# Optimization experiments

Measured on AMD Instinct MI355X. Metric: run time of the kernel, lower is better.

Reference implementation:

```python
import jax, jax.numpy as jnp
import numpy as np


def setup_inputs() -> dict:
    key = jax.random.key(0)
    ks = jax.random.split(key, 5)
    B, T, D, U = 32, 2048, 512, 512
    scale = 1.0 / np.sqrt(D)
    return {
        "full": jax.random.normal(ks[0], (B, T, D), jnp.float32),
        "last": jax.random.normal(ks[1], (B, D), jnp.float32),
        "W1": jax.random.normal(ks[2], (D, U), jnp.float32) * scale,
        "b1": jnp.zeros((U,), jnp.float32),
        "W2": jax.random.normal(ks[3], (D, U), jnp.float32) * scale,
        "b2": jnp.zeros((U,), jnp.float32),
        "V": jax.random.normal(ks[4], (U, 1), jnp.float32) * (1.0 / np.sqrt(U)),
        "bV": jnp.zeros((1,), jnp.float32),
    }


def reference(full, last, W1, b1, W2, b2, V, bV):
    # full: [B,T,D], last: [B,D]
    h1 = jnp.einsum("btd,du->btu", full, W1) + b1          # [B,T,U]
    h2 = last @ W2 + b2                                      # [B,U]
    score = jnp.tanh(h1 + h2[:, None, :]) @ V + bV           # [B,T,1]
    attn = jax.nn.softmax(score, axis=1)                     # [B,T,1]
    context = jnp.sum(attn * full, axis=1)                   # [B,D]
    return context
```

## Files before the change

### kernel.cpp

```cpp
#include <hip/hip_runtime.h>
#include <math.h>


#define BB 32
#define TT 2048
#define DD 512
#define UU 512
#define BKK 32
#define KSTEPS 16

typedef short bf16x8 __attribute__((ext_vector_type(8)));
typedef float f32x4  __attribute__((ext_vector_type(4)));

static __device__ __forceinline__ short f2bf(float f) {
    unsigned x = __float_as_uint(f);
    return (short)((x + 0x7fffu + ((x >> 16) & 1u)) >> 16);
}

static __device__ __forceinline__ float fast_tanh(float x) {
    float e = __expf(2.f * x);
    return 1.f - 2.f * __builtin_amdgcn_rcpf(e + 1.f);
}

__global__ __launch_bounds__(256) void prep_kernel(const float* __restrict__ W1,
                                                   short* __restrict__ W1T,
                                                   const float* __restrict__ last,
                                                   const float* __restrict__ W2,
                                                   const float* __restrict__ b1,
                                                   const float* __restrict__ b2,
                                                   float* __restrict__ h2) {
    __shared__ float tile[32][33];
    __shared__ float ls[DD];
    __shared__ float part[256];
    const int bid = blockIdx.x;
    const int tid = threadIdx.x;
    if (bid < 256) {
        const int tr = (bid >> 4) << 5;
        const int tc = (bid & 15) << 5;
#pragma unroll
        for (int p = 0; p < 4; ++p) {
            const int r = p * 8 + (tid >> 5), c = tid & 31;
            tile[r][c] = W1[(size_t)(tr + r) * UU + tc + c];
        }
        __syncthreads();
#pragma unroll
        for (int p = 0; p < 4; ++p) {
            const int r = p * 8 + (tid >> 5), c = tid & 31;
            W1T[(size_t)(tc + r) * DD + tr + c] = f2bf(tile[c][r]);
        }
    } else {
        const int b2i = bid - 256;
        const int b  = b2i >> 2;
        const int u0 = (b2i & 3) << 7;
        for (int i = tid; i < DD; i += 256) ls[i] = last[b * DD + i];
        __syncthreads();
        const int uu = tid & 127;
        const int dh = tid >> 7;
        float acc = 0.f;
#pragma unroll 8
        for (int d = dh * 256; d < dh * 256 + 256; ++d)
            acc += ls[d] * W2[d * UU + u0 + uu];
        part[tid] = acc;
        __syncthreads();
        if (tid < 128) {
            const int u = u0 + tid;
            h2[b * UU + u] = part[tid] + part[tid + 128] + b1[u] + b2[u];
        }
    }
}

__global__ __launch_bounds__(512) void score_kernel(const float* __restrict__ full,
                                                    const short* __restrict__ W1T,
                                                    const float* __restrict__ h2,
                                                    const float* __restrict__ V,
                                                    float* __restrict__ ctx,
                                                    float* __restrict__ m_arr,
                                                    float* __restrict__ l_arr) {
    __shared__ __align__(16) float a32[2][128 * BKK];
    __shared__ __align__(16) short blds[2][512 * BKK];
    __shared__ float red64[8][64];
    __shared__ float esc[128];
    __shared__ float sred[8];
    __shared__ __align__(16) float red4[4][128][4];

    const int bid = blockIdx.x;
    const int b    = bid >> 4;
    const int t0   = (bid & 15) << 7;
    const int tid  = threadIdx.x;
    const int w    = tid >> 6;
    const int lane = tid & 63;
    const int quad = lane >> 4;
    const int col  = lane & 15;
    const int wm   = w >> 2;
    const int wn   = w & 3;

    f32x4 acc[4][8];
#pragma unroll
    for (int i = 0; i < 4; ++i)
#pragma unroll
        for (int j = 0; j < 8; ++j) acc[i][j] = (f32x4){0.f, 0.f, 0.f, 0.f};

    const size_t fullbase = (size_t)(b * TT + t0) * DD;

#define STAGE(bufidx, koidx) do {                                                     \
        _Pragma("unroll")                                                             \
        for (int i = 0; i < 2; ++i) {                                                 \
            const int sb = w * 128 + i * 64;                                          \
            const int s  = sb + lane;                                                 \
            const int r  = s >> 3;                                                    \
            const int cc = (s & 7) ^ (r & 7);                                         \
            const float* g = &full[fullbase + (size_t)r * DD + (koidx) * BKK + cc * 4]; \
            __builtin_amdgcn_global_load_lds(                                         \
                (const __attribute__((address_space(1))) void*)g,                     \
                (__attribute__((address_space(3))) void*)&a32[bufidx][sb * 4], 16, 0, 0); \
        }                                                                             \
        _Pragma("unroll")                                                             \
        for (int i = 0; i < 4; ++i) {                                                 \
            const int sb = w * 256 + i * 64;                                          \
            const int s  = sb + lane;                                                 \
            const int u  = s >> 2;                                                    \
            const int kc = (s & 3) ^ ((u >> 1) & 3);                                  \
            const short* g = &W1T[(size_t)u * DD + (koidx) * BKK + kc * 8];           \
            __builtin_amdgcn_global_load_lds(                                         \
                (const __attribute__((address_space(1))) void*)g,                     \
                (__attribute__((address_space(3))) void*)&blds[bufidx][sb * 8], 16, 0, 0); \
        }                                                                             \
    } while (0)

    STAGE(0, 0);
    STAGE(1, 1);
    asm volatile("s_waitcnt vmcnt(6)" ::: "memory");
    __builtin_amdgcn_s_barrier();

    int cur = 0;
    for (int ko = 0; ko < KSTEPS; ++ko) {
        f32x4 alo[4], ahi[4];
        bf16x8 bfr[8];
#pragma unroll
        for (int mt = 0; mt < 4; ++mt) {
            const int r  = wm * 64 + mt * 16 + col;
            const int c0 = quad * 2;
            alo[mt] = *(const f32x4*)&a32[cur][(r * 8 + (c0 ^ (r & 7))) * 4];
            ahi[mt] = *(const f32x4*)&a32[cur][(r * 8 + ((c0 + 1) ^ (r & 7))) * 4];
        }
#pragma unroll
        for (int nt = 0; nt < 8; ++nt) {
            const int u = wn * 128 + nt * 16 + col;
            bfr[nt] = *(const bf16x8*)&blds[cur][(u * 4 + (quad ^ ((u >> 1) & 3))) * 8];
        }
        asm volatile("s_waitcnt lgkmcnt(0)" ::: "memory");
        __builtin_amdgcn_sched_barrier(0);
        __builtin_amdgcn_s_barrier();

        if (ko + 2 < KSTEPS) STAGE(cur, ko + 2);

        bf16x8 af[4];
#pragma unroll
        for (int mt = 0; mt < 4; ++mt)
            af[mt] = (bf16x8){f2bf(alo[mt].x), f2bf(alo[mt].y), f2bf(alo[mt].z), f2bf(alo[mt].w),
                              f2bf(ahi[mt].x), f2bf(ahi[mt].y), f2bf(ahi[mt].z), f2bf(ahi[mt].w)};
#pragma unroll
        for (int nt = 0; nt < 8; ++nt)
#pragma unroll
            for (int mt = 0; mt < 4; ++mt)
                acc[mt][nt] = __builtin_amdgcn_mfma_f32_16x16x32_bf16(af[mt], bfr[nt], acc[mt][nt], 0, 0, 0);

        if (ko < KSTEPS - 2) {
            asm volatile("s_waitcnt vmcnt(6)" ::: "memory");
        } else if (ko == KSTEPS - 2) {
            asm volatile("s_waitcnt vmcnt(0)" ::: "memory");
        }
        if (ko < KSTEPS - 1) __builtin_amdgcn_s_barrier();
        cur ^= 1;
    }
#undef STAGE

    float srow[16];
#pragma unroll
    for (int i = 0; i < 16; ++i) srow[i] = 0.f;
#pragma unroll
    for (int nt = 0; nt < 8; ++nt) {
        const int u = wn * 128 + nt * 16 + col;
        const float hv = h2[b * UU + u];
        const float vv = V[u];
#pragma unroll
        for (int mt = 0; mt < 4; ++mt)
#pragma unroll
            for (int r = 0; r < 4; ++r)
                srow[mt * 4 + r] += fast_tanh(acc[mt][nt][r] + hv) * vv;
    }
#pragma unroll
    for (int off = 1; off < 16; off <<= 1) {
#pragma unroll
        for (int i = 0; i < 16; ++i) srow[i] += __shfl_xor(srow[i], off, 64);
    }
    if (col == 0) {
#pragma unroll
        for (int mt = 0; mt < 4; ++mt)
#pragma unroll
            for (int r = 0; r < 4; ++r)
                red64[w][mt * 16 + quad * 4 + r] = srow[mt * 4 + r];
    }
    __syncthreads();

    float sv = 0.f;
    if (tid < 128) {
        const int wmX = tid >> 6, rr = tid & 63;
        sv = red64[wmX * 4 + 0][rr] + red64[wmX * 4 + 1][rr] +
             red64[wmX * 4 + 2][rr] + red64[wmX * 4 + 3][rr];
        float mv = sv;
#pragma unroll
        for (int off = 1; off < 64; off <<= 1) mv = fmaxf(mv, __shfl_xor(mv, off, 64));
        if (lane == 0) sred[w] = mv;
    }
    __syncthreads();
    const float M = fmaxf(sred[0], sred[1]);
    if (tid < 128) {
        float e = __expf(sv - M);
        esc[tid] = e;
#pragma unroll
        for (int off = 1; off < 64; off <<= 1) e += __shfl_xor(e, off, 64);
        if (lane == 0) sred[4 + w] = e;
    }
    __syncthreads();
    if (tid == 0) { m_arr[bid] = M; l_arr[bid] = sred[4] + sred[5]; }

    const int c  = tid & 127;
    const int tp = tid >> 7;
    float ax = 0.f, ay = 0.f, az = 0.f, aw = 0.f;
#pragma unroll 4
    for (int i = 0; i < 32; ++i) {
        const int t = i * 4 + tp;
        const float4 v = *(const float4*)&full[fullbase + (size_t)t * DD + c * 4];
        const float e = esc[t];
        ax += e * v.x; ay += e * v.y; az += e * v.z; aw += e * v.w;
    }
    *(float4*)&red4[tp][c][0] = make_float4(ax, ay, az, aw);
    __syncthreads();
    if (tp == 0) {
        const float4 p0 = *(const float4*)&red4[0][c][0];
        const float4 p1 = *(const float4*)&red4[1][c][0];
        const float4 p2 = *(const float4*)&red4[2][c][0];
        const float4 p3 = *(const float4*)&red4[3][c][0];
        float4 s = make_float4(p0.x + p1.x + p2.x + p3.x,
                               p0.y + p1.y + p2.y + p3.y,
                               p0.z + p1.z + p2.z + p3.z,
                               p0.w + p1.w + p2.w + p3.w);
        *(float4*)&ctx[(size_t)bid * DD + c * 4] = s;
    }
}

__global__ __launch_bounds__(256) void combine_kernel(const float* __restrict__ ctx,
                                                      const float* __restrict__ m_arr,
                                                      const float* __restrict__ l_arr,
                                                      float* __restrict__ out) {
    const int b = blockIdx.x;
    const int tid = threadIdx.x;
    __shared__ float wgt[16];
    __shared__ float linv;
    if (tid == 0) {
        float M = -1e30f;
#pragma unroll
        for (int i = 0; i < 16; ++i) M = fmaxf(M, m_arr[b * 16 + i]);
        float l = 0.f;
#pragma unroll
        for (int i = 0; i < 16; ++i) {
            wgt[i] = __expf(m_arr[b * 16 + i] - M);
            l += wgt[i] * l_arr[b * 16 + i];
        }
        linv = 1.f / l;
    }
    __syncthreads();
    float s0 = 0.f, s1 = 0.f;
#pragma unroll
    for (int i = 0; i < 16; ++i) {
        const float wi = wgt[i];
        const float* cp = &ctx[(size_t)(b * 16 + i) * DD + tid * 2];
        s0 += wi * cp[0];
        s1 += wi * cp[1];
    }
    out[b * DD + tid * 2]     = s0 * linv;
    out[b * DD + tid * 2 + 1] = s1 * linv;
}

extern "C" void kernel_launch(void* const* d_in, const int* in_sizes, int n_in,
                              void* d_out, int out_size, void* d_ws, size_t ws_size,
                              hipStream_t stream) {
    const float* full = (const float*)d_in[0];
    const float* last = (const float*)d_in[1];
    const float* W1   = (const float*)d_in[2];
    const float* b1   = (const float*)d_in[3];
    const float* W2   = (const float*)d_in[4];
    const float* b2   = (const float*)d_in[5];
    const float* V    = (const float*)d_in[6];

    float* out   = (float*)d_out;
    float* h2    = (float*)d_ws;
    float* m_arr = h2 + (size_t)BB * UU;
    float* l_arr = m_arr + 512;
    float* ctx   = l_arr + 512;
    short* W1T   = (short*)(ctx + (size_t)BB * 16 * DD);

    prep_kernel<<<384, 256, 0, stream>>>(W1, W1T, last, W2, b1, b2, h2);
    score_kernel<<<BB * 16, 512, 0, stream>>>(full, W1T, h2, V, ctx, m_arr, l_arr);
    combine_kernel<<<BB, 256, 0, stream>>>(ctx, m_arr, l_arr, out);
}
```

Measured before the change: 259.9 us.

## Use 1024-thread blocks with register-staged bf16 A tile conversion

Doubles the score kernel block to 16 waves, each owning a 64x64 output tile instead of 64x128. The A operand (full) is now loaded into registers, converted to bf16 once and written to LDS, rather than copied as fp32 via global_load_lds and converted per wave after the LDS read. The goal is to remove the redundant per-wave conversion, halve A-tile LDS traffic and raise occupancy. In exchange it adds VGPR pressure limits from launch_bounds(1024), more waitcnt and barrier coordination, and register-path global loads for A.

```diff
diff --git a/kernel.cpp b/kernel.cpp
--- a/kernel.cpp
+++ b/kernel.cpp
@@ -10,6 +10,7 @@
 #define KSTEPS 16
 
 typedef short bf16x8 __attribute__((ext_vector_type(8)));
+typedef short s16x4  __attribute__((ext_vector_type(4)));
 typedef float f32x4  __attribute__((ext_vector_type(4)));
 
 static __device__ __forceinline__ short f2bf(float f) {
@@ -69,19 +70,19 @@
     }
 }
 
-__global__ __launch_bounds__(512) void score_kernel(const float* __restrict__ full,
-                                                    const short* __restrict__ W1T,
-                                                    const float* __restrict__ h2,
-                                                    const float* __restrict__ V,
-                                                    float* __restrict__ ctx,
-                                                    float* __restrict__ m_arr,
-                                                    float* __restrict__ l_arr) {
-    __shared__ __align__(16) float a32[2][128 * BKK];
-    __shared__ __align__(16) short blds[2][512 * BKK];
-    __shared__ float red64[8][64];
+__global__ __launch_bounds__(1024, 4) void score_kernel(const float* __restrict__ full,
+                                                        const short* __restrict__ W1T,
+                                                        const float* __restrict__ h2,
+                                                        const float* __restrict__ V,
+                                                        float* __restrict__ ctx,
+                                                        float* __restrict__ m_arr,
+                                                        float* __restrict__ l_arr) {
+    __shared__ __align__(16) short a16[2][128 * 32];
+    __shared__ __align__(16) short blds[2][512 * 32];
+    __shared__ float red64[16][64];
     __shared__ float esc[128];
     __shared__ float sred[8];
-    __shared__ __align__(16) float red4[4][128][4];
+    __shared__ __align__(16) float red4[8][128][4];
 
     const int bid = blockIdx.x;
     const int b    = bid >> 4;
@@ -91,32 +92,26 @@
     const int lane = tid & 63;
     const int quad = lane >> 4;
     const int col  = lane & 15;
-    const int wm   = w >> 2;
-    const int wn   = w & 3;
-
-    f32x4 acc[4][8];
+    const int wm   = w >> 3;
+    const int wn   = w & 7;
+
+    f32x4 acc[4][4];
 #pragma unroll
     for (int i = 0; i < 4; ++i)
 #pragma unroll
-        for (int j = 0; j < 8; ++j) acc[i][j] = (f32x4){0.f, 0.f, 0.f, 0.f};
+        for (int j = 0; j < 4; ++j) acc[i][j] = (f32x4){0.f, 0.f, 0.f, 0.f};
 
     const size_t fullbase = (size_t)(b * TT + t0) * DD;
 
-#define STAGE(bufidx, koidx) do {                                                     \
+    const int sr = tid >> 3;
+    const int se = tid & 7;
+    const float* aSrc = &full[fullbase + (size_t)sr * DD + se * 4];
+    const int awOff = sr * 32 + ((((se >> 1) ^ (sr & 3)) << 3) + ((se & 1) << 2));
+
+#define STAGE_B(bufidx, koidx) do {                                                   \
         _Pragma("unroll")                                                             \
         for (int i = 0; i < 2; ++i) {                                                 \
             const int sb = w * 128 + i * 64;                                          \
-            const int s  = sb + lane;                                                 \
-            const int r  = s >> 3;                                                    \
-            const int cc = (s & 7) ^ (r & 7);                                         \
-            const float* g = &full[fullbase + (size_t)r * DD + (koidx) * BKK + cc * 4]; \
-            __builtin_amdgcn_global_load_lds(                                         \
-                (const __attribute__((address_space(1))) void*)g,                     \
-                (__attribute__((address_space(3))) void*)&a32[bufidx][sb * 4], 16, 0, 0); \
-        }                                                                             \
-        _Pragma("unroll")                                                             \
-        for (int i = 0; i < 4; ++i) {                                                 \
-            const int sb = w * 256 + i * 64;                                          \
             const int s  = sb + lane;                                                 \
             const int u  = s >> 2;                                                    \
             const int kc = (s & 3) ^ ((u >> 1) & 3);                                  \
@@ -127,60 +122,74 @@
         }                                                                             \
     } while (0)
 
-    STAGE(0, 0);
-    STAGE(1, 1);
-    asm volatile("s_waitcnt vmcnt(6)" ::: "memory");
+#define CVT_WRITE(buf, ar) do {                                                       \
+        s16x4 q_ = (s16x4){f2bf((ar).x), f2bf((ar).y), f2bf((ar).z), f2bf((ar).w)};   \
+        *(s16x4*)&a16[buf][awOff] = q_;                                               \
+    } while (0)
+
+    f32x4 aregA = *(const f32x4*)(aSrc + 0 * BKK);
+    f32x4 aregB = *(const f32x4*)(aSrc + 1 * BKK);
+    STAGE_B(0, 0);
+    STAGE_B(1, 1);
+    asm volatile("s_waitcnt vmcnt(5)" ::: "memory");
+    CVT_WRITE(0, aregA);
+    asm volatile("s_waitcnt vmcnt(2)" ::: "memory");
+    asm volatile("s_waitcnt lgkmcnt(0)" ::: "memory");
     __builtin_amdgcn_s_barrier();
 
-    int cur = 0;
     for (int ko = 0; ko < KSTEPS; ++ko) {
-        f32x4 alo[4], ahi[4];
-        bf16x8 bfr[8];
+        const int cur = ko & 1;
+        bf16x8 af[4], bfr[4];
 #pragma unroll
         for (int mt = 0; mt < 4; ++mt) {
-            const int r  = wm * 64 + mt * 16 + col;
-            const int c0 = quad * 2;
-            alo[mt] = *(const f32x4*)&a32[cur][(r * 8 + (c0 ^ (r & 7))) * 4];
-            ahi[mt] = *(const f32x4*)&a32[cur][(r * 8 + ((c0 + 1) ^ (r & 7))) * 4];
-        }
-#pragma unroll
-        for (int nt = 0; nt < 8; ++nt) {
-            const int u = wn * 128 + nt * 16 + col;
+            const int r = wm * 64 + mt * 16 + col;
+            af[mt] = *(const bf16x8*)&a16[cur][r * 32 + ((quad ^ (r & 3)) << 3)];
+        }
+#pragma unroll
+        for (int nt = 0; nt < 4; ++nt) {
+            const int u = wn * 64 + nt * 16 + col;
             bfr[nt] = *(const bf16x8*)&blds[cur][(u * 4 + (quad ^ ((u >> 1) & 3))) * 8];
         }
         asm volatile("s_waitcnt lgkmcnt(0)" ::: "memory");
         __builtin_amdgcn_sched_barrier(0);
         __builtin_amdgcn_s_barrier();
 
-        if (ko + 2 < KSTEPS) STAGE(cur, ko + 2);
-
-        bf16x8 af[4];
-#pragma unroll
-        for (int mt = 0; mt < 4; ++mt)
-            af[mt] = (bf16x8){f2bf(alo[mt].x), f2bf(alo[mt].y), f2bf(alo[mt].z), f2bf(alo[mt].w),
-                              f2bf(ahi[mt].x), f2bf(ahi[mt].y), f2bf(ahi[mt].z), f2bf(ahi[mt].w)};
-#pragma unroll
-        for (int nt = 0; nt < 8; ++nt)
+        if (ko + 1 < KSTEPS) {
+            asm volatile("s_waitcnt vmcnt(2)" ::: "memory");
+            if (ko & 1) CVT_WRITE(cur ^ 1, aregA);
+            else        CVT_WRITE(cur ^ 1, aregB);
+        }
+        if (ko + 2 < KSTEPS) {
+            if (ko & 1) aregB = *(const f32x4*)(aSrc + (ko + 2) * BKK);
+            else        aregA = *(const f32x4*)(aSrc + (ko + 2) * BKK);
+        }
+        if (ko + 2 < KSTEPS) STAGE_B(cur, ko + 2);
+
+#pragma unroll
+        for (int nt = 0; nt < 4; ++nt)
 #pragma unroll
             for (int mt = 0; mt < 4; ++mt)
                 acc[mt][nt] = __builtin_amdgcn_mfma_f32_16x16x32_bf16(af[mt], bfr[nt], acc[mt][nt], 0, 0, 0);
 
         if (ko < KSTEPS - 2) {
-            asm volatile("s_waitcnt vmcnt(6)" ::: "memory");
+            asm volatile("s_waitcnt vmcnt(3)" ::: "memory");
         } else if (ko == KSTEPS - 2) {
             asm volatile("s_waitcnt vmcnt(0)" ::: "memory");
         }
-        if (ko < KSTEPS - 1) __builtin_amdgcn_s_barrier();
-        cur ^= 1;
-    }
-#undef STAGE
+        if (ko < KSTEPS - 1) {
+            asm volatile("s_waitcnt lgkmcnt(0)" ::: "memory");
+            __builtin_amdgcn_s_barrier();
+        }
+    }
+#undef STAGE_B
+#undef CVT_WRITE
 
     float srow[16];
 #pragma unroll
     for (int i = 0; i < 16; ++i) srow[i] = 0.f;
 #pragma unroll
-    for (int nt = 0; nt < 8; ++nt) {
-        const int u = wn * 128 + nt * 16 + col;
+    for (int nt = 0; nt < 4; ++nt) {
+        const int u = wn * 64 + nt * 16 + col;
         const float hv = h2[b * UU + u];
         const float vv = V[u];
 #pragma unroll
@@ -206,8 +215,8 @@
     float sv = 0.f;
     if (tid < 128) {
         const int wmX = tid >> 6, rr = tid & 63;
-        sv = red64[wmX * 4 + 0][rr] + red64[wmX * 4 + 1][rr] +
-             red64[wmX * 4 + 2][rr] + red64[wmX * 4 + 3][rr];
+#pragma unroll
+        for (int j = 0; j < 8; ++j) sv += red64[wmX * 8 + j][rr];
         float mv = sv;
 #pragma unroll
         for (int off = 1; off < 64; off <<= 1) mv = fmaxf(mv, __shfl_xor(mv, off, 64));
@@ -229,8 +238,8 @@
     const int tp = tid >> 7;
     float ax = 0.f, ay = 0.f, az = 0.f, aw = 0.f;
 #pragma unroll 4
-    for (int i = 0; i < 32; ++i) {
-        const int t = i * 4 + tp;
+    for (int i = 0; i < 16; ++i) {
+        const int t = i * 8 + tp;
         const float4 v = *(const float4*)&full[fullbase + (size_t)t * DD + c * 4];
         const float e = esc[t];
         ax += e * v.x; ay += e * v.y; az += e * v.z; aw += e * v.w;
@@ -238,14 +247,12 @@
     *(float4*)&red4[tp][c][0] = make_float4(ax, ay, az, aw);
     __syncthreads();
     if (tp == 0) {
-        const float4 p0 = *(const float4*)&red4[0][c][0];
-        const float4 p1 = *(const float4*)&red4[1][c][0];
-        const float4 p2 = *(const float4*)&red4[2][c][0];
-        const float4 p3 = *(const float4*)&red4[3][c][0];
-        float4 s = make_float4(p0.x + p1.x + p2.x + p3.x,
-                               p0.y + p1.y + p2.y + p3.y,
-                               p0.z + p1.z + p2.z + p3.z,
-                               p0.w + p1.w + p2.w + p3.w);
+        float4 s = make_float4(0.f, 0.f, 0.f, 0.f);
+#pragma unroll
+        for (int j = 0; j < 8; ++j) {
+            const float4 p = *(const float4*)&red4[j][c][0];
+            s.x += p.x; s.y += p.y; s.z += p.z; s.w += p.w;
+        }
         *(float4*)&ctx[(size_t)bid * DD + c * 4] = s;
     }
 }
@@ -302,6 +309,6 @@
     short* W1T   = (short*)(ctx + (size_t)BB * 16 * DD);
 
     prep_kernel<<<384, 256, 0, stream>>>(W1, W1T, last, W2, b1, b2, h2);
-    score_kernel<<<BB * 16, 512, 0, stream>>>(full, W1T, h2, V, ctx, m_arr, l_arr);
+    score_kernel<<<BB * 16, 1024, 0, stream>>>(full, W1T, h2, V, ctx, m_arr, l_arr);
     combine_kernel<<<BB, 256, 0, stream>>>(ctx, m_arr, l_arr, out);
 }
```

New measurement: 266.7 us. 2.6% more time.

## Split score GEMM k-step into phases interleaving staged loads with MFMA

Applied to the files above, without the earlier changes.

The main loop of the score kernel is restructured into three phases per k-step. Each phase reads only part of the B fragments, issues the prefetch of A and then B for step k+2 between MFMA groups, and raises wave priority with s_setprio around the MFMA bursts. Shared memory becomes one flat buffer, with the reduction scratch aliased onto the B staging region. The aim is to hide global-to-LDS transfers and LDS reads behind matrix math. It costs extra barriers per iteration, and the reuse of staging memory for reductions depends on the final barrier placement being correct.

```diff
diff --git a/kernel.cpp b/kernel.cpp
--- a/kernel.cpp
+++ b/kernel.cpp
@@ -76,14 +76,15 @@
                                                     float* __restrict__ ctx,
                                                     float* __restrict__ m_arr,
                                                     float* __restrict__ l_arr) {
-    __shared__ __align__(16) float a32[2][128 * BKK];
-    __shared__ __align__(16) short blds[2][512 * BKK];
-    __shared__ float red64[8][64];
-    __shared__ float esc[128];
-    __shared__ float sred[8];
-    __shared__ __align__(16) float red4[4][128][4];
-
-    const int bid = blockIdx.x;
+    __shared__ __align__(16) char smem[98304];
+    float* a32  = (float*)smem;
+    short* blds = (short*)(smem + 32768);
+    float (*red64)[64]    = (float(*)[64])(smem + 32768);
+    float* esc            = (float*)(smem + 32768 + 2048);
+    float* sred           = (float*)(smem + 32768 + 2560);
+    float (*red4)[128][4] = (float(*)[128][4])(smem + 32768 + 4096);
+
+    const int bid  = blockIdx.x;
     const int b    = bid >> 4;
     const int t0   = (bid & 15) << 7;
     const int tid  = threadIdx.x;
@@ -94,86 +95,119 @@
     const int wm   = w >> 2;
     const int wn   = w & 3;
 
+    const size_t fullbase = (size_t)(b * TT + t0) * DD;
+
     f32x4 acc[4][8];
 #pragma unroll
     for (int i = 0; i < 4; ++i)
 #pragma unroll
         for (int j = 0; j < 8; ++j) acc[i][j] = (f32x4){0.f, 0.f, 0.f, 0.f};
 
-    const size_t fullbase = (size_t)(b * TT + t0) * DD;
-
-#define STAGE(bufidx, koidx) do {                                                     \
+#define STAGE_A(bufidx, koidx) do {                                                   \
         _Pragma("unroll")                                                             \
         for (int i = 0; i < 2; ++i) {                                                 \
-            const int sb = w * 128 + i * 64;                                          \
-            const int s  = sb + lane;                                                 \
+            const int s  = i * 512 + w * 64 + lane;                                   \
             const int r  = s >> 3;                                                    \
             const int cc = (s & 7) ^ (r & 7);                                         \
             const float* g = &full[fullbase + (size_t)r * DD + (koidx) * BKK + cc * 4]; \
             __builtin_amdgcn_global_load_lds(                                         \
                 (const __attribute__((address_space(1))) void*)g,                     \
-                (__attribute__((address_space(3))) void*)&a32[bufidx][sb * 4], 16, 0, 0); \
+                (__attribute__((address_space(3))) void*)&a32[(bufidx) * 4096 + s * 4], 16, 0, 0); \
         }                                                                             \
+    } while (0)
+
+#define STAGE_B(bufidx, koidx) do {                                                   \
         _Pragma("unroll")                                                             \
         for (int i = 0; i < 4; ++i) {                                                 \
-            const int sb = w * 256 + i * 64;                                          \
-            const int s  = sb + lane;                                                 \
+            const int s  = i * 512 + w * 64 + lane;                                   \
             const int u  = s >> 2;                                                    \
             const int kc = (s & 3) ^ ((u >> 1) & 3);                                  \
             const short* g = &W1T[(size_t)u * DD + (koidx) * BKK + kc * 8];           \
             __builtin_amdgcn_global_load_lds(                                         \
                 (const __attribute__((address_space(1))) void*)g,                     \
-                (__attribute__((address_space(3))) void*)&blds[bufidx][sb * 8], 16, 0, 0); \
+                (__attribute__((address_space(3))) void*)&blds[(bufidx) * 16384 + s * 8], 16, 0, 0); \
         }                                                                             \
     } while (0)
 
-    STAGE(0, 0);
-    STAGE(1, 1);
-    asm volatile("s_waitcnt vmcnt(6)" ::: "memory");
+    STAGE_A(0, 0);
+    STAGE_A(1, 1);
+    STAGE_B(0, 0);
+    STAGE_B(1, 1);
+    asm volatile("s_waitcnt vmcnt(4)" ::: "memory");
     __builtin_amdgcn_s_barrier();
 
-    int cur = 0;
     for (int ko = 0; ko < KSTEPS; ++ko) {
+        const int cur = ko & 1;
+        const int abase = cur * 4096;
+        const int bbase = cur * 16384;
+
         f32x4 alo[4], ahi[4];
-        bf16x8 bfr[8];
+        bf16x8 bfrA[4];
 #pragma unroll
         for (int mt = 0; mt < 4; ++mt) {
             const int r  = wm * 64 + mt * 16 + col;
             const int c0 = quad * 2;
-            alo[mt] = *(const f32x4*)&a32[cur][(r * 8 + (c0 ^ (r & 7))) * 4];
-            ahi[mt] = *(const f32x4*)&a32[cur][(r * 8 + ((c0 + 1) ^ (r & 7))) * 4];
-        }
-#pragma unroll
-        for (int nt = 0; nt < 8; ++nt) {
+            alo[mt] = *(const f32x4*)&a32[abase + (r * 8 + (c0 ^ (r & 7))) * 4];
+            ahi[mt] = *(const f32x4*)&a32[abase + (r * 8 + ((c0 + 1) ^ (r & 7))) * 4];
+        }
+#pragma unroll
+        for (int nt = 0; nt < 4; ++nt) {
             const int u = wn * 128 + nt * 16 + col;
-            bfr[nt] = *(const bf16x8*)&blds[cur][(u * 4 + (quad ^ ((u >> 1) & 3))) * 8];
+            bfrA[nt] = *(const bf16x8*)&blds[bbase + (u * 4 + (quad ^ ((u >> 1) & 3))) * 8];
         }
         asm volatile("s_waitcnt lgkmcnt(0)" ::: "memory");
         __builtin_amdgcn_sched_barrier(0);
-        __builtin_amdgcn_s_barrier();
-
-        if (ko + 2 < KSTEPS) STAGE(cur, ko + 2);
-
         bf16x8 af[4];
 #pragma unroll
         for (int mt = 0; mt < 4; ++mt)
             af[mt] = (bf16x8){f2bf(alo[mt].x), f2bf(alo[mt].y), f2bf(alo[mt].z), f2bf(alo[mt].w),
                               f2bf(ahi[mt].x), f2bf(ahi[mt].y), f2bf(ahi[mt].z), f2bf(ahi[mt].w)};
-#pragma unroll
-        for (int nt = 0; nt < 8; ++nt)
-#pragma unroll
-            for (int mt = 0; mt < 4; ++mt)
-                acc[mt][nt] = __builtin_amdgcn_mfma_f32_16x16x32_bf16(af[mt], bfr[nt], acc[mt][nt], 0, 0, 0);
-
-        if (ko < KSTEPS - 2) {
+        __builtin_amdgcn_s_setprio(1);
+#pragma unroll
+        for (int mt = 0; mt < 4; ++mt) {
+            acc[mt][0] = __builtin_amdgcn_mfma_f32_16x16x32_bf16(af[mt], bfrA[0], acc[mt][0], 0, 0, 0);
+            acc[mt][1] = __builtin_amdgcn_mfma_f32_16x16x32_bf16(af[mt], bfrA[1], acc[mt][1], 0, 0, 0);
+        }
+        __builtin_amdgcn_s_setprio(0);
+        __builtin_amdgcn_s_barrier();
+
+        bf16x8 bfrB[4];
+#pragma unroll
+        for (int nt = 0; nt < 4; ++nt) {
+            const int u = wn * 128 + (nt + 4) * 16 + col;
+            bfrB[nt] = *(const bf16x8*)&blds[bbase + (u * 4 + (quad ^ ((u >> 1) & 3))) * 8];
+        }
+        if (ko + 2 < KSTEPS) STAGE_A(cur, ko + 2);
+        asm volatile("s_waitcnt lgkmcnt(0)" ::: "memory");
+        __builtin_amdgcn_sched_barrier(0);
+        __builtin_amdgcn_s_setprio(1);
+#pragma unroll
+        for (int mt = 0; mt < 4; ++mt) {
+            acc[mt][2] = __builtin_amdgcn_mfma_f32_16x16x32_bf16(af[mt], bfrA[2], acc[mt][2], 0, 0, 0);
+            acc[mt][3] = __builtin_amdgcn_mfma_f32_16x16x32_bf16(af[mt], bfrA[3], acc[mt][3], 0, 0, 0);
+        }
+        __builtin_amdgcn_s_setprio(0);
+        __builtin_amdgcn_s_barrier();
+
+        if (ko + 2 < KSTEPS) STAGE_B(cur, ko + 2);
+        __builtin_amdgcn_s_setprio(1);
+#pragma unroll
+        for (int mt = 0; mt < 4; ++mt) {
+            acc[mt][4] = __builtin_amdgcn_mfma_f32_16x16x32_bf16(af[mt], bfrB[0], acc[mt][4], 0, 0, 0);
+            acc[mt][5] = __builtin_amdgcn_mfma_f32_16x16x32_bf16(af[mt], bfrB[1], acc[mt][5], 0, 0, 0);
+            acc[mt][6] = __builtin_amdgcn_mfma_f32_16x16x32_bf16(af[mt], bfrB[2], acc[mt][6], 0, 0, 0);
+            acc[mt][7] = __builtin_amdgcn_mfma_f32_16x16x32_bf16(af[mt], bfrB[3], acc[mt][7], 0, 0, 0);
+        }
+        __builtin_amdgcn_s_setprio(0);
+        if (ko <= KSTEPS - 3) {
             asm volatile("s_waitcnt vmcnt(6)" ::: "memory");
         } else if (ko == KSTEPS - 2) {
             asm volatile("s_waitcnt vmcnt(0)" ::: "memory");
         }
-        if (ko < KSTEPS - 1) __builtin_amdgcn_s_barrier();
-        cur ^= 1;
-    }
-#undef STAGE
+        __builtin_amdgcn_s_barrier();
+    }
+#undef STAGE_A
+#undef STAGE_B
 
     float srow[16];
 #pragma unroll
```

New measurement: 260.8 us. Within noise of the previous version (+0.3%).
